# Kernel tuning notes

Hardware: AMD Instinct MI355X
Metric: run time of the kernel (lower is better)

## Reference

```python
import jax, jax.numpy as jnp
import numpy as np

EPS = 1e-6

def feature_map(x):
    # 'elu' feature map: elu(x) + 1 (positive feature map from Katharopoulos et al.)
    return jax.nn.elu(x) + 1.0

def setup_inputs() -> dict:
    key = jax.random.key(0)
    kq, kk, kv = jax.random.split(key, 3)
    B, L, H, D = 4, 2048, 16, 64
    q = jax.random.normal(kq, (B, L, H, D), dtype=jnp.float32)
    k = jax.random.normal(kk, (B, L, H, D), dtype=jnp.float32)
    v = jax.random.normal(kv, (B, L, H, D), dtype=jnp.float32)
    return {"q": q, "k": k, "v": v}

def reference(q, k, v):
    # q, k, v: [N, L, H, D]  (attention_mask=None -> causal linear attention)
    qf = feature_map(q)
    kf = feature_map(k)
    # normalizer: z[n,l,h] = sum_d qf[n,l,h,d] * cumsum_s<=l kf[n,s,h,d]
    z = jnp.einsum('nlhd,nlhd->nlh', qf, jnp.cumsum(kf, axis=1)) + EPS
    # causal_dot_product via scan over sequence with carry S[n,h,d,m]
    B, L, H, D = q.shape
    M = v.shape[-1]
    qs = jnp.moveaxis(qf, 1, 0)  # [L, N, H, D]
    ks = jnp.moveaxis(kf, 1, 0)
    vs = jnp.moveaxis(v, 1, 0)

    def step(S, qkv):
        ql, kl, vl = qkv                              # [N,H,D], [N,H,D], [N,H,M]
        S = S + jnp.einsum('nhd,nhm->nhdm', kl, vl)   # running sum of k v^T
        out = jnp.einsum('nhd,nhdm->nhm', ql, S)
        return S, out

    S0 = jnp.zeros((B, H, D, M), dtype=q.dtype)
    _, outs = jax.lax.scan(step, S0, (qs, ks, vs))    # outs: [L, N, H, M]
    v_ = jnp.moveaxis(outs, 0, 1)                     # [N, L, H, M]
    return v_ / z[..., None]
```

## Files before the change

kernel.cpp:

```cpp
#include <hip/hip_runtime.h>
#include <cstdint>

#define LL 2048
#define HH 16
#define DD 64
#define NC 32
#define LSTR 1024
#define EPSF 1e-6f
#define PAD 72

typedef __bf16 bf16x8 __attribute__((ext_vector_type(8)));
typedef float floatx4 __attribute__((ext_vector_type(4)));
typedef unsigned short ushortx8 __attribute__((ext_vector_type(8)));
typedef unsigned short ushortx4 __attribute__((ext_vector_type(4)));

static __device__ __forceinline__ float fmap(float x){ return x > 0.f ? x + 1.f : __expf(x); }
static __device__ __forceinline__ unsigned short f2bf(float f){
    unsigned u = __builtin_bit_cast(unsigned, f);
    u += 0x7fffu + ((u >> 16) & 1u);
    return (unsigned short)(u >> 16);
}
static __device__ __forceinline__ float bf2f(unsigned short s){
    unsigned u = ((unsigned)s) << 16;
    return __builtin_bit_cast(float, u);
}
static __device__ __forceinline__ bf16x8 ldf(const unsigned short* p){
    return __builtin_bit_cast(bf16x8, *(const ushortx8*)p);
}

__global__ __launch_bounds__(256) void k1(const float* __restrict__ kp, const float* __restrict__ vp,
                                          unsigned short* __restrict__ kvt, float* __restrict__ ks)
{
    __shared__ __align__(16) unsigned short kft[DD*PAD];
    __shared__ __align__(16) unsigned short vts[DD*PAD];
    const int ci = blockIdx.x;
    const int c = ci & 31, bh = ci >> 5, b = bh >> 4, h = bh & 15;
    const int t = threadIdx.x;
    const int64_t gbase = ((int64_t)(b*LL + c*DD)*HH + h)*DD;
#pragma unroll
    for (int i = 0; i < 4; ++i) {
        int flat = t + 256*i;
        int l = flat >> 4, col = (flat & 15) << 2;
        float4 kq = *(const float4*)(kp + gbase + (int64_t)l*LSTR + col);
        float4 vq = *(const float4*)(vp + gbase + (int64_t)l*LSTR + col);
        kft[(col+0)*PAD + l] = f2bf(fmap(kq.x));
        kft[(col+1)*PAD + l] = f2bf(fmap(kq.y));
        kft[(col+2)*PAD + l] = f2bf(fmap(kq.z));
        kft[(col+3)*PAD + l] = f2bf(fmap(kq.w));
        vts[(col+0)*PAD + l] = f2bf(vq.x);
        vts[(col+1)*PAD + l] = f2bf(vq.y);
        vts[(col+2)*PAD + l] = f2bf(vq.z);
        vts[(col+3)*PAD + l] = f2bf(vq.w);
    }
    __syncthreads();
    const int w = t >> 6, lane = t & 63, quad = lane >> 4, lr = lane & 15;
    const int m0 = 16*w;
    floatx4 acc[4];
#pragma unroll
    for (int dt = 0; dt < 4; ++dt) acc[dt] = floatx4{0.f,0.f,0.f,0.f};
#pragma unroll
    for (int kk = 0; kk < 2; ++kk) {
        bf16x8 a = ldf(vts + (m0+lr)*PAD + kk*32 + quad*8);
#pragma unroll
        for (int dt = 0; dt < 4; ++dt) {
            bf16x8 bb = ldf(kft + (dt*16+lr)*PAD + kk*32 + quad*8);
            acc[dt] = __builtin_amdgcn_mfma_f32_16x16x32_bf16(a, bb, acc[dt], 0, 0, 0);
        }
    }
    unsigned short* kvo = kvt + (int64_t)ci*4096;
#pragma unroll
    for (int dt = 0; dt < 4; ++dt)
#pragma unroll
        for (int r = 0; r < 4; ++r)
            kvo[(m0 + quad*4 + r)*DD + dt*16 + lr] = f2bf(acc[dt][r]);
    if (t < DD) {
        float s = 0.f;
#pragma unroll
        for (int j = 0; j < 8; ++j) {
            ushortx8 u = *(const ushortx8*)(kft + t*PAD + j*8);
#pragma unroll
            for (int e = 0; e < 8; ++e) s += bf2f(u[e]);
        }
        ks[(int64_t)ci*DD + t] = s;
    }
}

__global__ __launch_bounds__(256) void k2(unsigned short* __restrict__ kvt, float* __restrict__ ks)
{
    const int blk = blockIdx.x;
    const int bh = blk >> 1, half = blk & 1, t = threadIdx.x;
    const int g8 = half*256 + t;
    unsigned short* base = kvt + (int64_t)bh*NC*4096 + g8*8;
    float run[8] = {0,0,0,0,0,0,0,0};
    ushortx8 x = *(const ushortx8*)(base);
    for (int c = 0; c < NC-1; ++c) {
        ushortx8 xn = *(const ushortx8*)(base + (int64_t)(c+1)*4096);
        ushortx8 o;
#pragma unroll
        for (int e = 0; e < 8; ++e) { o[e] = f2bf(run[e]); run[e] += bf2f(x[e]); }
        *(ushortx8*)(base + (int64_t)c*4096) = o;
        x = xn;
    }
    {
        ushortx8 o;
#pragma unroll
        for (int e = 0; e < 8; ++e) o[e] = f2bf(run[e]);
        *(ushortx8*)(base + (int64_t)(NC-1)*4096) = o;
    }
    if (half == 0 && t < DD) {
        float r = 0.f;
        float* kb = ks + (int64_t)bh*NC*DD + t;
        for (int c = 0; c < NC; ++c) { float xx = kb[(int64_t)c*DD]; kb[(int64_t)c*DD] = r; r += xx; }
    }
}

__global__ __launch_bounds__(256) void k3(const float* __restrict__ qp, const float* __restrict__ kp,
                                          const float* __restrict__ vp,
                                          const unsigned short* __restrict__ kvt,
                                          const float* __restrict__ ks, float* __restrict__ outp)
{
    __shared__ __align__(16) unsigned short qf [DD*PAD];
    __shared__ __align__(16) unsigned short kfx[80*PAD];
    __shared__ __align__(16) unsigned short vts[DD*PAD];
    __shared__ __align__(16) unsigned short stp[DD*PAD];
    __shared__ __align__(16) unsigned short asx[DD*PAD];
    __shared__ float zr[DD];
    const int ci = blockIdx.x;
    const int c = ci & 31, bh = ci >> 5, b = bh >> 4, h = bh & 15;
    const int t = threadIdx.x;
    const int64_t gbase = ((int64_t)(b*LL + c*DD)*HH + h)*DD;
    const unsigned short* kvg = kvt + (int64_t)ci*4096;
    const float* ksg = ks + (int64_t)ci*DD;
#pragma unroll
    for (int i = 0; i < 4; ++i) {
        int flat = t + 256*i;
        int l = flat >> 4, col = (flat & 15) << 2;
        float4 qq = *(const float4*)(qp + gbase + (int64_t)l*LSTR + col);
        float4 kq = *(const float4*)(kp + gbase + (int64_t)l*LSTR + col);
        float4 vq = *(const float4*)(vp + gbase + (int64_t)l*LSTR + col);
        ushortx4 qb = { f2bf(fmap(qq.x)), f2bf(fmap(qq.y)), f2bf(fmap(qq.z)), f2bf(fmap(qq.w)) };
        ushortx4 kb = { f2bf(fmap(kq.x)), f2bf(fmap(kq.y)), f2bf(fmap(kq.z)), f2bf(fmap(kq.w)) };
        *(ushortx4*)(qf  + l*PAD + col) = qb;
        *(ushortx4*)(kfx + l*PAD + col) = kb;
        vts[(col+0)*PAD + l] = f2bf(vq.x);
        vts[(col+1)*PAD + l] = f2bf(vq.y);
        vts[(col+2)*PAD + l] = f2bf(vq.z);
        vts[(col+3)*PAD + l] = f2bf(vq.w);
    }
#pragma unroll
    for (int i = 0; i < 2; ++i) {
        int g = t + 256*i;
        int m = g >> 3, off = (g & 7) << 3;
        *(ushortx8*)(stp + m*PAD + off) = *(const ushortx8*)(kvg + g*8);
    }
    if (t < 135) *(ushortx8*)(kfx + 65*PAD + t*8) = ushortx8{0,0,0,0,0,0,0,0};
    if (t < DD)  kfx[64*PAD + t] = f2bf(ksg[t]);
    __syncthreads();

    const int w = t >> 6, lane = t & 63, quad = lane >> 4, lr = lane & 15;
    const int l0 = 16*w;
    bf16x8 aq[2];
    aq[0] = ldf(qf + (l0+lr)*PAD + quad*8);
    aq[1] = ldf(qf + (l0+lr)*PAD + 32 + quad*8);
    floatx4 sc[5];
#pragma unroll
    for (int tt = 0; tt < 5; ++tt) sc[tt] = floatx4{0.f,0.f,0.f,0.f};
#pragma unroll
    for (int kk = 0; kk < 2; ++kk)
#pragma unroll
        for (int tt = 0; tt < 5; ++tt) {
            bf16x8 bb = ldf(kfx + (tt*16+lr)*PAD + kk*32 + quad*8);
            sc[tt] = __builtin_amdgcn_mfma_f32_16x16x32_bf16(aq[kk], bb, sc[tt], 0, 0, 0);
        }
    float zp[4] = {0.f,0.f,0.f,0.f};
#pragma unroll
    for (int tt = 0; tt < 4; ++tt)
#pragma unroll
        for (int r = 0; r < 4; ++r) {
            int row = l0 + quad*4 + r;
            int col = tt*16 + lr;
            float val = (col <= row) ? sc[tt][r] : 0.f;
            zp[r] += val;
            asx[row*PAD + col] = f2bf(val);
        }
#pragma unroll
    for (int r = 0; r < 4; ++r) zp[r] += (lr == 0) ? sc[4][r] : 0.f;
#pragma unroll
    for (int m = 1; m < 16; m <<= 1)
#pragma unroll
        for (int r = 0; r < 4; ++r) zp[r] += __shfl_xor(zp[r], m, 64);
    if (lr == 0)
#pragma unroll
        for (int r = 0; r < 4; ++r) zr[l0 + quad*4 + r] = 1.f / (zp[r] + EPSF);
    __syncthreads();

    floatx4 oa[4];
#pragma unroll
    for (int mt = 0; mt < 4; ++mt) oa[mt] = floatx4{0.f,0.f,0.f,0.f};
#pragma unroll
    for (int kk = 0; kk < 2; ++kk) {
        bf16x8 a2 = ldf(asx + (l0+lr)*PAD + kk*32 + quad*8);
#pragma unroll
        for (int mt = 0; mt < 4; ++mt) {
            bf16x8 bv = ldf(vts + (mt*16+lr)*PAD + kk*32 + quad*8);
            oa[mt] = __builtin_amdgcn_mfma_f32_16x16x32_bf16(a2, bv, oa[mt], 0, 0, 0);
        }
    }
#pragma unroll
    for (int kk = 0; kk < 2; ++kk)
#pragma unroll
        for (int mt = 0; mt < 4; ++mt) {
            bf16x8 bs = ldf(stp + (mt*16+lr)*PAD + kk*32 + quad*8);
            oa[mt] = __builtin_amdgcn_mfma_f32_16x16x32_bf16(aq[kk], bs, oa[mt], 0, 0, 0);
        }
#pragma unroll
    for (int r = 0; r < 4; ++r) {
        int row = l0 + quad*4 + r;
        float rz = zr[row];
#pragma unroll
        for (int mt = 0; mt < 4; ++mt)
            outp[gbase + (int64_t)row*LSTR + mt*16 + lr] = oa[mt][r] * rz;
    }
}

extern "C" void kernel_launch(void* const* d_in, const int* in_sizes, int n_in,
                              void* d_out, int out_size, void* d_ws, size_t ws_size,
                              hipStream_t stream) {
    const float* q = (const float*)d_in[0];
    const float* k = (const float*)d_in[1];
    const float* v = (const float*)d_in[2];
    float* out = (float*)d_out;
    unsigned short* kvt = (unsigned short*)d_ws;
    float* ks = (float*)((char*)d_ws + (size_t)2048*4096*2);
    k1<<<2048, 256, 0, stream>>>(k, v, kvt, ks);
    k2<<<128,  256, 0, stream>>>(kvt, ks);
    k3<<<2048, 256, 0, stream>>>(q, k, v, kvt, ks, out);
}
```

Before: 157.7 us.

## Cut LDS footprint in k3, widen k2 parallelism, vectorize LDS staging stores

In k3, Q is loaded straight from global memory into MFMA registers instead of being staged through shared memory. The state matrix S is read directly from global memory, and the kfx buffer is reused for the masked score matrix. This cuts shared memory from five tiles to two, aiming for higher occupancy. V is now stored row-major with vector stores, and the transposed fragments are gathered with scalar LDS reads at use time, in both k1 and k3. k2 is split into 512 blocks that each handle 2 elements per thread, exposing more parallelism in the chunk prefix scan. The trade-offs are more scalar LDS reads, uncached global reads of S inside the MFMA loop, and an extra barrier.

```diff
diff --git a/kernel.cpp b/kernel.cpp
--- a/kernel.cpp
+++ b/kernel.cpp
@@ -13,6 +13,7 @@
 typedef float floatx4 __attribute__((ext_vector_type(4)));
 typedef unsigned short ushortx8 __attribute__((ext_vector_type(8)));
 typedef unsigned short ushortx4 __attribute__((ext_vector_type(4)));
+typedef unsigned short ushortx2 __attribute__((ext_vector_type(2)));
 
 static __device__ __forceinline__ float fmap(float x){ return x > 0.f ? x + 1.f : __expf(x); }
 static __device__ __forceinline__ unsigned short f2bf(float f){
@@ -32,25 +33,28 @@
                                           unsigned short* __restrict__ kvt, float* __restrict__ ks)
 {
     __shared__ __align__(16) unsigned short kft[DD*PAD];
-    __shared__ __align__(16) unsigned short vts[DD*PAD];
+    __shared__ __align__(16) unsigned short v_s[DD*PAD];
     const int ci = blockIdx.x;
     const int c = ci & 31, bh = ci >> 5, b = bh >> 4, h = bh & 15;
     const int t = threadIdx.x;
     const int64_t gbase = ((int64_t)(b*LL + c*DD)*HH + h)*DD;
 #pragma unroll
-    for (int i = 0; i < 4; ++i) {
+    for (int i = 0; i < 2; ++i) {
         int flat = t + 256*i;
-        int l = flat >> 4, col = (flat & 15) << 2;
-        float4 kq = *(const float4*)(kp + gbase + (int64_t)l*LSTR + col);
-        float4 vq = *(const float4*)(vp + gbase + (int64_t)l*LSTR + col);
-        kft[(col+0)*PAD + l] = f2bf(fmap(kq.x));
-        kft[(col+1)*PAD + l] = f2bf(fmap(kq.y));
-        kft[(col+2)*PAD + l] = f2bf(fmap(kq.z));
-        kft[(col+3)*PAD + l] = f2bf(fmap(kq.w));
-        vts[(col+0)*PAD + l] = f2bf(vq.x);
-        vts[(col+1)*PAD + l] = f2bf(vq.y);
-        vts[(col+2)*PAD + l] = f2bf(vq.z);
-        vts[(col+3)*PAD + l] = f2bf(vq.w);
+        int l0 = (flat >> 4) * 2, col = (flat & 15) << 2;
+        const float* g0 = kp + gbase + (int64_t)l0*LSTR + col;
+        float4 ka = *(const float4*)(g0);
+        float4 kb = *(const float4*)(g0 + LSTR);
+        unsigned short ua[4] = { f2bf(fmap(ka.x)), f2bf(fmap(ka.y)), f2bf(fmap(ka.z)), f2bf(fmap(ka.w)) };
+        unsigned short ub[4] = { f2bf(fmap(kb.x)), f2bf(fmap(kb.y)), f2bf(fmap(kb.z)), f2bf(fmap(kb.w)) };
+#pragma unroll
+        for (int e = 0; e < 4; ++e)
+            *(ushortx2*)(kft + (col+e)*PAD + l0) = ushortx2{ ua[e], ub[e] };
+        const float* v0 = vp + gbase + (int64_t)l0*LSTR + col;
+        float4 va = *(const float4*)(v0);
+        float4 vb = *(const float4*)(v0 + LSTR);
+        *(ushortx4*)(v_s + l0*PAD + col)     = ushortx4{ f2bf(va.x), f2bf(va.y), f2bf(va.z), f2bf(va.w) };
+        *(ushortx4*)(v_s + (l0+1)*PAD + col) = ushortx4{ f2bf(vb.x), f2bf(vb.y), f2bf(vb.z), f2bf(vb.w) };
     }
     __syncthreads();
     const int w = t >> 6, lane = t & 63, quad = lane >> 4, lr = lane & 15;
@@ -60,7 +64,11 @@
     for (int dt = 0; dt < 4; ++dt) acc[dt] = floatx4{0.f,0.f,0.f,0.f};
 #pragma unroll
     for (int kk = 0; kk < 2; ++kk) {
-        bf16x8 a = ldf(vts + (m0+lr)*PAD + kk*32 + quad*8);
+        ushortx8 u;
+#pragma unroll
+        for (int j = 0; j < 8; ++j)
+            u[j] = v_s[(kk*32 + quad*8 + j)*PAD + m0 + lr];
+        bf16x8 a = __builtin_bit_cast(bf16x8, u);
 #pragma unroll
         for (int dt = 0; dt < 4; ++dt) {
             bf16x8 bb = ldf(kft + (dt*16+lr)*PAD + kk*32 + quad*8);
@@ -88,26 +96,20 @@
 __global__ __launch_bounds__(256) void k2(unsigned short* __restrict__ kvt, float* __restrict__ ks)
 {
     const int blk = blockIdx.x;
-    const int bh = blk >> 1, half = blk & 1, t = threadIdx.x;
-    const int g8 = half*256 + t;
-    unsigned short* base = kvt + (int64_t)bh*NC*4096 + g8*8;
-    float run[8] = {0,0,0,0,0,0,0,0};
-    ushortx8 x = *(const ushortx8*)(base);
+    const int bh = blk >> 3, part = blk & 7, t = threadIdx.x;
+    unsigned short* base = kvt + (int64_t)bh*NC*4096 + (part*256 + t)*2;
+    float r0 = 0.f, r1 = 0.f;
+    unsigned x = *(const unsigned*)base;
     for (int c = 0; c < NC-1; ++c) {
-        ushortx8 xn = *(const ushortx8*)(base + (int64_t)(c+1)*4096);
-        ushortx8 o;
-#pragma unroll
-        for (int e = 0; e < 8; ++e) { o[e] = f2bf(run[e]); run[e] += bf2f(x[e]); }
-        *(ushortx8*)(base + (int64_t)c*4096) = o;
+        unsigned xn = *(const unsigned*)(base + (int64_t)(c+1)*4096);
+        unsigned o = (unsigned)f2bf(r0) | ((unsigned)f2bf(r1) << 16);
+        r0 += bf2f((unsigned short)(x & 0xffffu));
+        r1 += bf2f((unsigned short)(x >> 16));
+        *(unsigned*)(base + (int64_t)c*4096) = o;
         x = xn;
     }
-    {
-        ushortx8 o;
-#pragma unroll
-        for (int e = 0; e < 8; ++e) o[e] = f2bf(run[e]);
-        *(ushortx8*)(base + (int64_t)(NC-1)*4096) = o;
-    }
-    if (half == 0 && t < DD) {
+    *(unsigned*)(base + (int64_t)(NC-1)*4096) = (unsigned)f2bf(r0) | ((unsigned)f2bf(r1) << 16);
+    if (part == 0 && t < DD) {
         float r = 0.f;
         float* kb = ks + (int64_t)bh*NC*DD + t;
         for (int c = 0; c < NC; ++c) { float xx = kb[(int64_t)c*DD]; kb[(int64_t)c*DD] = r; r += xx; }
@@ -119,11 +121,8 @@
                                           const unsigned short* __restrict__ kvt,
                                           const float* __restrict__ ks, float* __restrict__ outp)
 {
-    __shared__ __align__(16) unsigned short qf [DD*PAD];
     __shared__ __align__(16) unsigned short kfx[80*PAD];
-    __shared__ __align__(16) unsigned short vts[DD*PAD];
-    __shared__ __align__(16) unsigned short stp[DD*PAD];
-    __shared__ __align__(16) unsigned short asx[DD*PAD];
+    __shared__ __align__(16) unsigned short v_s[DD*PAD];
     __shared__ float zr[DD];
     const int ci = blockIdx.x;
     const int c = ci & 31, bh = ci >> 5, b = bh >> 4, h = bh & 15;
@@ -135,33 +134,28 @@
     for (int i = 0; i < 4; ++i) {
         int flat = t + 256*i;
         int l = flat >> 4, col = (flat & 15) << 2;
-        float4 qq = *(const float4*)(qp + gbase + (int64_t)l*LSTR + col);
         float4 kq = *(const float4*)(kp + gbase + (int64_t)l*LSTR + col);
         float4 vq = *(const float4*)(vp + gbase + (int64_t)l*LSTR + col);
-        ushortx4 qb = { f2bf(fmap(qq.x)), f2bf(fmap(qq.y)), f2bf(fmap(qq.z)), f2bf(fmap(qq.w)) };
-        ushortx4 kb = { f2bf(fmap(kq.x)), f2bf(fmap(kq.y)), f2bf(fmap(kq.z)), f2bf(fmap(kq.w)) };
-        *(ushortx4*)(qf  + l*PAD + col) = qb;
-        *(ushortx4*)(kfx + l*PAD + col) = kb;
-        vts[(col+0)*PAD + l] = f2bf(vq.x);
-        vts[(col+1)*PAD + l] = f2bf(vq.y);
-        vts[(col+2)*PAD + l] = f2bf(vq.z);
-        vts[(col+3)*PAD + l] = f2bf(vq.w);
-    }
-#pragma unroll
-    for (int i = 0; i < 2; ++i) {
-        int g = t + 256*i;
-        int m = g >> 3, off = (g & 7) << 3;
-        *(ushortx8*)(stp + m*PAD + off) = *(const ushortx8*)(kvg + g*8);
+        *(ushortx4*)(kfx + l*PAD + col) = ushortx4{ f2bf(fmap(kq.x)), f2bf(fmap(kq.y)), f2bf(fmap(kq.z)), f2bf(fmap(kq.w)) };
+        *(ushortx4*)(v_s + l*PAD + col) = ushortx4{ f2bf(vq.x), f2bf(vq.y), f2bf(vq.z), f2bf(vq.w) };
     }
     if (t < 135) *(ushortx8*)(kfx + 65*PAD + t*8) = ushortx8{0,0,0,0,0,0,0,0};
     if (t < DD)  kfx[64*PAD + t] = f2bf(ksg[t]);
-    __syncthreads();
 
     const int w = t >> 6, lane = t & 63, quad = lane >> 4, lr = lane & 15;
     const int l0 = 16*w;
     bf16x8 aq[2];
-    aq[0] = ldf(qf + (l0+lr)*PAD + quad*8);
-    aq[1] = ldf(qf + (l0+lr)*PAD + 32 + quad*8);
+#pragma unroll
+    for (int kk = 0; kk < 2; ++kk) {
+        const float* g = qp + gbase + (int64_t)(l0+lr)*LSTR + kk*32 + quad*8;
+        float4 x0 = *(const float4*)(g);
+        float4 x1 = *(const float4*)(g + 4);
+        ushortx8 u = { f2bf(fmap(x0.x)), f2bf(fmap(x0.y)), f2bf(fmap(x0.z)), f2bf(fmap(x0.w)),
+                       f2bf(fmap(x1.x)), f2bf(fmap(x1.y)), f2bf(fmap(x1.z)), f2bf(fmap(x1.w)) };
+        aq[kk] = __builtin_bit_cast(bf16x8, u);
+    }
+    __syncthreads();
+
     floatx4 sc[5];
 #pragma unroll
     for (int tt = 0; tt < 5; ++tt) sc[tt] = floatx4{0.f,0.f,0.f,0.f};
@@ -172,6 +166,8 @@
             bf16x8 bb = ldf(kfx + (tt*16+lr)*PAD + kk*32 + quad*8);
             sc[tt] = __builtin_amdgcn_mfma_f32_16x16x32_bf16(aq[kk], bb, sc[tt], 0, 0, 0);
         }
+    __syncthreads();
+
     float zp[4] = {0.f,0.f,0.f,0.f};
 #pragma unroll
     for (int tt = 0; tt < 4; ++tt)
@@ -181,7 +177,7 @@
             int col = tt*16 + lr;
             float val = (col <= row) ? sc[tt][r] : 0.f;
             zp[r] += val;
-            asx[row*PAD + col] = f2bf(val);
+            kfx[row*PAD + col] = f2bf(val);
         }
 #pragma unroll
     for (int r = 0; r < 4; ++r) zp[r] += (lr == 0) ? sc[4][r] : 0.f;
@@ -192,17 +188,20 @@
     if (lr == 0)
 #pragma unroll
         for (int r = 0; r < 4; ++r) zr[l0 + quad*4 + r] = 1.f / (zp[r] + EPSF);
-    __syncthreads();
 
     floatx4 oa[4];
 #pragma unroll
     for (int mt = 0; mt < 4; ++mt) oa[mt] = floatx4{0.f,0.f,0.f,0.f};
 #pragma unroll
     for (int kk = 0; kk < 2; ++kk) {
-        bf16x8 a2 = ldf(asx + (l0+lr)*PAD + kk*32 + quad*8);
+        bf16x8 a2 = ldf(kfx + (l0+lr)*PAD + kk*32 + quad*8);
 #pragma unroll
         for (int mt = 0; mt < 4; ++mt) {
-            bf16x8 bv = ldf(vts + (mt*16+lr)*PAD + kk*32 + quad*8);
+            ushortx8 uv;
+#pragma unroll
+            for (int j = 0; j < 8; ++j)
+                uv[j] = v_s[(kk*32 + quad*8 + j)*PAD + mt*16 + lr];
+            bf16x8 bv = __builtin_bit_cast(bf16x8, uv);
             oa[mt] = __builtin_amdgcn_mfma_f32_16x16x32_bf16(a2, bv, oa[mt], 0, 0, 0);
         }
     }
@@ -210,7 +209,7 @@
     for (int kk = 0; kk < 2; ++kk)
 #pragma unroll
         for (int mt = 0; mt < 4; ++mt) {
-            bf16x8 bs = ldf(stp + (mt*16+lr)*PAD + kk*32 + quad*8);
+            bf16x8 bs = ldf(kvg + (mt*16+lr)*64 + kk*32 + quad*8);
             oa[mt] = __builtin_amdgcn_mfma_f32_16x16x32_bf16(aq[kk], bs, oa[mt], 0, 0, 0);
         }
 #pragma unroll
@@ -233,6 +232,6 @@
     unsigned short* kvt = (unsigned short*)d_ws;
     float* ks = (float*)((char*)d_ws + (size_t)2048*4096*2);
     k1<<<2048, 256, 0, stream>>>(k, v, kvt, ks);
-    k2<<<128,  256, 0, stream>>>(kvt, ks);
+    k2<<<512,  256, 0, stream>>>(kvt, ks);
     k3<<<2048, 256, 0, stream>>>(q, k, v, kvt, ks, out);
 }
```

Measured after the change: 157.7 us. No clear change (+0.0%).
